# Kernel optimization log

Measured on AMD Instinct MI355X. Metric: run time of the kernel, lower is better.

The kernel has to match this reference:

```python
import jax, jax.numpy as jnp
import numpy as np

B, D = 65536, 512
EPS = 1e-15
MAXN = 1.0 - 4e-3  # geoopt fp32 ball boundary, c = 1


def _norm(x):
    return jnp.sqrt(jnp.clip(jnp.sum(x * x, -1, keepdims=True), EPS))


def _artanh(x):
    return jnp.arctanh(jnp.clip(x, -1.0 + 1e-7, 1.0 - 1e-7))


def projx(x):
    n = _norm(x)
    return jnp.where(n > MAXN, x / n * MAXN, x)


def mobius_add(x, y):
    x2 = jnp.sum(x * x, -1, keepdims=True)
    y2 = jnp.sum(y * y, -1, keepdims=True)
    xy = jnp.sum(x * y, -1, keepdims=True)
    num = (1.0 + 2.0 * xy + y2) * x + (1.0 - x2) * y
    den = 1.0 + 2.0 * xy + x2 * y2
    return num / jnp.maximum(den, EPS)


def expmap(x, u):
    un = _norm(u)
    lam = 2.0 / jnp.maximum(1.0 - jnp.sum(x * x, -1, keepdims=True), EPS)
    return mobius_add(x, jnp.tanh(lam * un / 2.0) * u / un)


def logmap(x, y):
    sub = mobius_add(-x, y)
    sn = _norm(sub)
    lam = 2.0 / jnp.maximum(1.0 - jnp.sum(x * x, -1, keepdims=True), EPS)
    return (2.0 / lam) * _artanh(sn) * sub / sn


def expmap0(u):
    un = _norm(u)
    return jnp.tanh(un) * u / un


def logmap0(y):
    yn = _norm(y)
    return _artanh(yn) * y / yn


def mobius_scalar_mul(r, x):
    xn = _norm(x)
    return jnp.tanh(r * _artanh(xn)) * x / xn


def poincare_fc(x, z, bias):
    # HNN++ Poincare fully-connected layer, c = 1
    zn = jnp.sqrt(jnp.clip(jnp.sum(z * z, 0), EPS))   # [out]
    z_unit = z / zn                                   # [in, out]
    two_r = 2.0 * bias                                # [out]
    cx2 = jnp.sum(x * x, -1, keepdims=True)           # [B, 1]
    inner = x @ z_unit                                # [B, out]
    v = 2.0 * zn * jnp.arcsinh(
        (2.0 * inner * jnp.cosh(two_r) - (1.0 + cx2) * jnp.sinh(two_r))
        / jnp.maximum(1.0 - cx2, EPS))
    w = jnp.sinh(v)
    return w / (1.0 + jnp.sqrt(1.0 + jnp.sum(w * w, -1, keepdims=True)))


def setup_inputs():
    key = jax.random.key(0)
    k1, k2, k3 = jax.random.split(key, 3)
    u1 = jax.random.normal(k1, (B, D), jnp.float32)
    u2 = jax.random.normal(k2, (B, D), jnp.float32)
    # points strictly inside the unit Poincare ball
    x_current = 0.7 * u1 / (1.0 + _norm(u1))
    x_previous = 0.7 * u2 / (1.0 + _norm(u2))
    # PoincareLinear id_init: 0.5*I, plus tiny noise so grads/outputs are non-degenerate
    z = 0.5 * jnp.eye(D, dtype=jnp.float32) + 0.01 * jax.random.normal(k3, (D, D), jnp.float32)
    bias = jnp.zeros((D,), jnp.float32)
    alpha = jnp.asarray(0.7, jnp.float32)
    step_size = jnp.asarray(1.0, jnp.float32)
    return {"x_current": x_current, "x_previous": x_previous, "z": z,
            "bias": bias, "alpha": alpha, "step_size": step_size}


def reference(x_current, x_previous, z, bias, alpha, step_size):
    # backward trajectory via logmap on the manifold (x_previous given)
    bt = logmap(x_previous, x_current)
    step = jax.nn.sigmoid(step_size)
    # PoincareLinear: expmap0 -> poincare_fc -> logmap0
    vel = logmap0(poincare_fc(expmap0(bt), z, bias))
    x_update = projx(expmap(x_current, step * vel))
    a = jax.nn.sigmoid(alpha)
    # poincare_residual_update
    xc = projx(x_current)
    xu = projx(x_update)
    x_next = projx(mobius_add(mobius_scalar_mul(a, xc), mobius_scalar_mul(1.0 - a, xu)))
    return (x_next, xc)
```

## Files before the change

### kernel.cpp

```cpp
#include <hip/hip_runtime.h>
#include <stdint.h>

#define DDIM 512
#define BROWS 65536
#define EPSF 1e-15f
#define MAXNF 0.996f
#define SQRT_EPSF 3.1622776e-8f
#define ATANH_CLIP 0.99999988f

typedef __bf16 bf16x8 __attribute__((ext_vector_type(8)));
typedef float f32x4 __attribute__((ext_vector_type(4)));

__device__ __forceinline__ unsigned short f2bf(float f) {
    union { float f; uint32_t u; } c; c.f = f;
    uint32_t u = c.u;
    u += 0x7fffu + ((u >> 16) & 1u);
    return (unsigned short)(u >> 16);
}

__device__ __forceinline__ float wred(float v) {
    v += __shfl_xor(v, 1);
    v += __shfl_xor(v, 2);
    v += __shfl_xor(v, 4);
    v += __shfl_xor(v, 8);
    v += __shfl_xor(v, 16);
    v += __shfl_xor(v, 32);
    return v;
}

__device__ __forceinline__ float fast_asinh(float t) {
    return __logf(t + sqrtf(fmaf(t, t, 1.0f)));
}
__device__ __forceinline__ float fast_sinh(float v) {
    float q = __expf(v);
    return 0.5f * (q - __builtin_amdgcn_rcpf(q));
}

__global__ void prep_kernel(const float* __restrict__ z, const float* __restrict__ bias,
                            float* __restrict__ znf, float* __restrict__ chv,
                            float* __restrict__ shv, unsigned short* __restrict__ zT) {
    int j = blockIdx.x;
    int l = threadIdx.x;
    float zv[8];
    float s = 0.f;
#pragma unroll
    for (int t = 0; t < 8; ++t) {
        float v = z[(size_t)(t * 64 + l) * DDIM + j];
        zv[t] = v;
        s = fmaf(v, v, s);
    }
    s = wred(s);
    float zn = sqrtf(fmaxf(s, EPSF));
    float inv = 1.0f / zn;
#pragma unroll
    for (int t = 0; t < 8; ++t)
        zT[(size_t)j * DDIM + t * 64 + l] = f2bf(zv[t] * inv);
    if (l == 0) {
        znf[j] = zn;
        float tr = 2.0f * bias[j];
        chv[j] = coshf(tr);
        shv[j] = sinhf(tr);
    }
}

__global__ __launch_bounds__(512, 2) void hpd_main(
    const float* __restrict__ Xc, const float* __restrict__ Xp,
    const float* __restrict__ znf, const float* __restrict__ chv, const float* __restrict__ shv,
    const unsigned short* __restrict__ zT,
    const float* __restrict__ alpha_p, const float* __restrict__ step_p,
    float* __restrict__ out)
{
    __shared__ __align__(16) unsigned char smem[98816];
    unsigned char* zbuf = smem + 65536;
    float* scx2 = (float*)(smem + 98304);
    float* sdcc = (float*)(smem + 98560);

    const int t = threadIdx.x;
    const int w = t >> 6;
    const int l = t & 63;
    const int l15 = l & 15;
    const int quad = l >> 4;
    const int r0 = blockIdx.x * 64;
    const size_t BDo = (size_t)BROWS * DDIM;

    float a_sig = 1.0f / (1.0f + __expf(-alpha_p[0]));
    float step_sig = 1.0f / (1.0f + __expf(-step_p[0]));

    float xcreg[8][8];
#pragma unroll
    for (int idx = 0; idx < 8; ++idx) {
        int row = (idx < 4) ? (w * 4 + idx) : (32 + w * 4 + (idx - 4));
        const float4* pc = (const float4*)(Xc + (size_t)(r0 + row) * DDIM + l * 8);
        const float4* pp = (const float4*)(Xp + (size_t)(r0 + row) * DDIM + l * 8);
        float4 c0 = pc[0], c1 = pc[1];
        float4 p0 = pp[0], p1 = pp[1];
        float xcv[8] = {c0.x, c0.y, c0.z, c0.w, c1.x, c1.y, c1.z, c1.w};
        float xpv[8] = {p0.x, p0.y, p0.z, p0.w, p1.x, p1.y, p1.z, p1.w};
        float dcc = 0.f, dpp = 0.f, dpc = 0.f;
#pragma unroll
        for (int j = 0; j < 8; ++j) {
            dcc = fmaf(xcv[j], xcv[j], dcc);
            dpp = fmaf(xpv[j], xpv[j], dpp);
            dpc = fmaf(xpv[j], xcv[j], dpc);
        }
        dcc = wred(dcc); dpp = wred(dpp); dpc = wred(dpc);
        float Ca = -(1.0f - 2.0f * dpc + dcc);
        float Cb = 1.0f - dpp;
        float den = fmaxf(1.0f - 2.0f * dpc + dpp * dcc, EPSF);
        float ssub = (Ca * Ca * dpp + 2.0f * Ca * Cb * dpc + Cb * Cb * dcc) / (den * den);
        float sn = sqrtf(fmaxf(ssub, EPSF));
        float tol = fmaxf(1.0f - dpp, EPSF);
        float art = atanhf(fminf(sn, ATANH_CLIP));
        float sbt = tol * art / sn;
        float un = fmaxf(tol * art, SQRT_EPSF);
        float te = tanhf(un);
        float se = te / un * sbt;
        float cep = se * Ca / den;
        float cex = se * Cb / den;
        if (l == 0) { scx2[row] = te * te; sdcc[row] = dcc; }
        unsigned short e8[8];
#pragma unroll
        for (int j = 0; j < 8; ++j) {
            e8[j] = f2bf(fmaf(cex, xcv[j], cep * xpv[j]));
            xcreg[idx][j] = xcv[j];
        }
        uint32_t u0 = (uint32_t)e8[0] | ((uint32_t)e8[1] << 16);
        uint32_t u1 = (uint32_t)e8[2] | ((uint32_t)e8[3] << 16);
        uint32_t u2 = (uint32_t)e8[4] | ((uint32_t)e8[5] << 16);
        uint32_t u3 = (uint32_t)e8[6] | ((uint32_t)e8[7] << 16);
        uint32_t off = row * 1024 + ((l ^ (row & 7)) * 16);
        *(uint4*)(smem + off) = make_uint4(u0, u1, u2, u3);
    }
    __syncthreads();

    f32x4 acc[4][4];
#pragma unroll
    for (int m = 0; m < 4; ++m)
#pragma unroll
        for (int j = 0; j < 4; ++j)
            acc[m][j] = (f32x4){0.f, 0.f, 0.f, 0.f};

#pragma unroll 1
    for (int ks = 0; ks < 16; ++ks) {
#pragma unroll
        for (int j = 0; j < 4; ++j) {
            int q = j * 512 + t;
            int n = q >> 2, c = q & 3;
            uint4 d = *(const uint4*)((const unsigned char*)zT + n * 1024 + ks * 64 + c * 16);
            int g = n >> 2;
            uint32_t off = g * 256 + (n & 3) * 16 + (((c + g) & 3) * 64);
            *(uint4*)(zbuf + off) = d;
        }
        __syncthreads();
        bf16x8 af[4], bfr[4];
#pragma unroll
        for (int m = 0; m < 4; ++m) {
            int row = m * 16 + l15;
            uint32_t off = row * 1024 + (((ks * 4 + quad) ^ (row & 7)) * 16);
            af[m] = *(const bf16x8*)(smem + off);
        }
#pragma unroll
        for (int j = 0; j < 4; ++j) {
            int n = w * 64 + j * 16 + l15;
            uint32_t off = (n >> 2) * 256 + (n & 3) * 16 + (((quad + (n >> 2)) & 3) * 64);
            bfr[j] = *(const bf16x8*)(zbuf + off);
        }
#pragma unroll
        for (int m = 0; m < 4; ++m)
#pragma unroll
            for (int j = 0; j < 4; ++j)
                acc[m][j] = __builtin_amdgcn_mfma_f32_16x16x32_bf16(af[m], bfr[j], acc[m][j], 0, 0, 0);
        __syncthreads();
    }

    float* stage = (float*)smem;
#pragma unroll
    for (int h = 0; h < 2; ++h) {
        __syncthreads();
#pragma unroll
        for (int mm = 0; mm < 2; ++mm) {
            int m = 2 * h + mm;
#pragma unroll
            for (int j = 0; j < 4; ++j) {
#pragma unroll
                for (int r = 0; r < 4; ++r) {
                    int rowl = mm * 16 + quad * 4 + r;
                    int n = w * 64 + j * 16 + l15;
                    stage[rowl * 512 + n] = acc[m][j][r];
                }
            }
        }
        __syncthreads();
#pragma unroll
        for (int i = 0; i < 4; ++i) {
            int rowl = w * 4 + i;
            int row = h * 32 + rowl;
            int idx = h * 4 + i;
            int grow = r0 + row;
            float4 in0 = *(const float4*)(stage + rowl * 512 + l * 8);
            float4 in1 = *(const float4*)(stage + rowl * 512 + l * 8 + 4);
            float inr[8] = {in0.x, in0.y, in0.z, in0.w, in1.x, in1.y, in1.z, in1.w};
            float4 zn0 = *(const float4*)(znf + l * 8);
            float4 zn1 = *(const float4*)(znf + l * 8 + 4);
            float4 ch0 = *(const float4*)(chv + l * 8);
            float4 ch1 = *(const float4*)(chv + l * 8 + 4);
            float4 sh0 = *(const float4*)(shv + l * 8);
            float4 sh1 = *(const float4*)(shv + l * 8 + 4);
            float znv[8] = {zn0.x, zn0.y, zn0.z, zn0.w, zn1.x, zn1.y, zn1.z, zn1.w};
            float chvv[8] = {ch0.x, ch0.y, ch0.z, ch0.w, ch1.x, ch1.y, ch1.z, ch1.w};
            float shvv[8] = {sh0.x, sh0.y, sh0.z, sh0.w, sh1.x, sh1.y, sh1.z, sh1.w};
            float cx2 = scx2[row], dcc = sdcc[row];
            float inv1m = 1.0f / fmaxf(1.0f - cx2, EPSF);
            float opc = 1.0f + cx2;
            float wv[8];
            float sw = 0.f, cw = 0.f;
#pragma unroll
            for (int j = 0; j < 8; ++j) {
                float arg = (2.0f * inr[j] * chvv[j] - opc * shvv[j]) * inv1m;
                float v = 2.0f * znv[j] * fast_asinh(arg);
                wv[j] = fast_sinh(v);
                sw = fmaf(wv[j], wv[j], sw);
                cw = fmaf(xcreg[idx][j], wv[j], cw);
            }
            sw = wred(sw); cw = wred(cw);
            float is = 1.0f / (1.0f + sqrtf(1.0f + sw));
            float nfc = sqrtf(fmaxf(sw * is * is, EPSF));
            float artf = atanhf(fminf(nfc, ATANH_CLIP));
            float un2 = fmaxf(step_sig * artf, SQRT_EPSF);
            float g = tanhf(un2 / fmaxf(1.0f - dcc, EPSF));
            float by = g * is / nfc;
            float xy = by * cw;
            float y2 = by * by * sw;
            float P = 1.0f + 2.0f * xy + y2;
            float den2 = fmaxf(1.0f + 2.0f * xy + dcc * y2, EPSF);
            float a1 = P / den2;
            float b1 = (1.0f - dcc) * by / den2;
            float s2u = a1 * a1 * dcc + 2.0f * a1 * b1 * cw + b1 * b1 * sw;
            float nxu = sqrtf(fmaxf(s2u, EPSF));
            float pj = (nxu > MAXNF) ? (MAXNF / nxu) : 1.0f;
            a1 *= pj; b1 *= pj;
            float nxu2 = fminf(nxu, MAXNF);
            float nx = sqrtf(fmaxf(dcc, EPSF));
            float sxc = (nx > MAXNF) ? (MAXNF / nx) : 1.0f;
            float nxc = fminf(nx, MAXNF);
            float A1 = tanhf(a_sig * atanhf(fminf(nxc, ATANH_CLIP))) / nxc * sxc;
            float t2s = tanhf((1.0f - a_sig) * atanhf(fminf(nxu2, ATANH_CLIP)));
            float sm2 = t2s / fmaxf(nxu2, SQRT_EPSF);
            float A2 = sm2 * a1, B2 = sm2 * b1;
            float x2m = A1 * A1 * dcc;
            float y2m = A2 * A2 * dcc + 2.0f * A2 * B2 * cw + B2 * B2 * sw;
            float xym = A1 * (A2 * dcc + B2 * cw);
            float num1 = 1.0f + 2.0f * xym + y2m;
            float num2 = 1.0f - x2m;
            float den3 = fmaxf(1.0f + 2.0f * xym + x2m * y2m, EPSF);
            float an = (num1 * A1 + num2 * A2) / den3;
            float bn = (num2 * B2) / den3;
            float s2n = an * an * dcc + 2.0f * an * bn * cw + bn * bn * sw;
            float nn = sqrtf(fmaxf(s2n, EPSF));
            float pj2 = (nn > MAXNF) ? (MAXNF / nn) : 1.0f;
            an *= pj2; bn *= pj2;
            float o0[8], o1[8];
#pragma unroll
            for (int j = 0; j < 8; ++j) {
                o0[j] = fmaf(an, xcreg[idx][j], bn * wv[j]);
                o1[j] = sxc * xcreg[idx][j];
            }
            float* p0 = out + (size_t)grow * DDIM + l * 8;
            float* p1 = out + BDo + (size_t)grow * DDIM + l * 8;
            *(float4*)(p0) = make_float4(o0[0], o0[1], o0[2], o0[3]);
            *(float4*)(p0 + 4) = make_float4(o0[4], o0[5], o0[6], o0[7]);
            *(float4*)(p1) = make_float4(o1[0], o1[1], o1[2], o1[3]);
            *(float4*)(p1 + 4) = make_float4(o1[4], o1[5], o1[6], o1[7]);
        }
    }
}

extern "C" void kernel_launch(void* const* d_in, const int* in_sizes, int n_in,
                              void* d_out, int out_size, void* d_ws, size_t ws_size,
                              hipStream_t stream) {
    const float* xc = (const float*)d_in[0];
    const float* xp = (const float*)d_in[1];
    const float* z = (const float*)d_in[2];
    const float* bias = (const float*)d_in[3];
    const float* alpha = (const float*)d_in[4];
    const float* stepsz = (const float*)d_in[5];
    float* out = (float*)d_out;

    float* znf = (float*)d_ws;
    float* chv = znf + 512;
    float* shv = znf + 1024;
    unsigned short* zT = (unsigned short*)(znf + 1536);

    prep_kernel<<<512, 64, 0, stream>>>(z, bias, znf, chv, shv, zT);
    hpd_main<<<BROWS / 64, 512, 0, stream>>>(xc, xp, znf, chv, shv, zT, alpha, stepsz, out);
}
```

Before: 631.9 us.

## Restructure epilogue in MFMA layout, load weights directly, drop z staging and registers

Drops the per-k-step shared-memory staging of the weight tile and its barriers, so each wave reads its bf16 B fragments straight from global (L2-resident) memory. The epilogue now works directly in the MFMA accumulator layout: row sums are reduced per wave, combined across waves in shared memory, and the per-row scalar math is done by 64 threads. Instead of holding x_current in registers, the epilogue re-reads it from global memory with strided scalar accesses, and the xc output is written early in the prologue. Fast tanh/atanh/reciprocal intrinsics replace the libm calls. Smaller LDS and fewer registers allow raising launch bounds to four blocks per CU. The trade-off is uncoalesced 4-byte global loads and stores in the epilogue, plus repeated global reads of z.

```diff
diff --git a/kernel.cpp b/kernel.cpp
--- a/kernel.cpp
+++ b/kernel.cpp
@@ -17,6 +17,8 @@
     u += 0x7fffu + ((u >> 16) & 1u);
     return (unsigned short)(u >> 16);
 }
+
+__device__ __forceinline__ float rcpf(float x) { return __builtin_amdgcn_rcpf(x); }
 
 __device__ __forceinline__ float wred(float v) {
     v += __shfl_xor(v, 1);
@@ -28,12 +30,21 @@
     return v;
 }
 
+__device__ __forceinline__ float fast_tanh_pos(float x) {
+    float t = __expf(-2.0f * x);
+    return (1.0f - t) * rcpf(1.0f + t);
+}
+__device__ __forceinline__ float fast_atanh_pos(float x) {
+    return 0.5f * __logf((1.0f + x) * rcpf(1.0f - x));
+}
 __device__ __forceinline__ float fast_asinh(float t) {
-    return __logf(t + sqrtf(fmaf(t, t, 1.0f)));
+    float a = fabsf(t);
+    float r = __logf(a + sqrtf(fmaf(a, a, 1.0f)));
+    return copysignf(r, t);
 }
 __device__ __forceinline__ float fast_sinh(float v) {
     float q = __expf(v);
-    return 0.5f * (q - __builtin_amdgcn_rcpf(q));
+    return 0.5f * (q - rcpf(q));
 }
 
 __global__ void prep_kernel(const float* __restrict__ z, const float* __restrict__ bias,
@@ -63,17 +74,20 @@
     }
 }
 
-__global__ __launch_bounds__(512, 2) void hpd_main(
+__global__ __launch_bounds__(512, 4) void hpd_main(
     const float* __restrict__ Xc, const float* __restrict__ Xp,
     const float* __restrict__ znf, const float* __restrict__ chv, const float* __restrict__ shv,
     const unsigned short* __restrict__ zT,
     const float* __restrict__ alpha_p, const float* __restrict__ step_p,
     float* __restrict__ out)
 {
-    __shared__ __align__(16) unsigned char smem[98816];
-    unsigned char* zbuf = smem + 65536;
-    float* scx2 = (float*)(smem + 98304);
-    float* sdcc = (float*)(smem + 98560);
+    __shared__ __align__(16) unsigned char smem[70656];
+    float* cx2s = (float*)(smem + 65536);
+    float* dccs = (float*)(smem + 65792);
+    float* swp  = (float*)(smem + 66048);
+    float* cwp  = (float*)(smem + 68096);
+    float* ans  = (float*)(smem + 70144);
+    float* bns  = (float*)(smem + 70400);
 
     const int t = threadIdx.x;
     const int w = t >> 6;
@@ -81,19 +95,19 @@
     const int l15 = l & 15;
     const int quad = l >> 4;
     const int r0 = blockIdx.x * 64;
-    const size_t BDo = (size_t)BROWS * DDIM;
-
-    float a_sig = 1.0f / (1.0f + __expf(-alpha_p[0]));
-    float step_sig = 1.0f / (1.0f + __expf(-step_p[0]));
-
-    float xcreg[8][8];
+
+    float a_sig = rcpf(1.0f + __expf(-alpha_p[0]));
+    float step_sig = rcpf(1.0f + __expf(-step_p[0]));
+
+    float* out1 = out + (size_t)BROWS * DDIM;
+
 #pragma unroll
     for (int idx = 0; idx < 8; ++idx) {
-        int row = (idx < 4) ? (w * 4 + idx) : (32 + w * 4 + (idx - 4));
-        const float4* pc = (const float4*)(Xc + (size_t)(r0 + row) * DDIM + l * 8);
-        const float4* pp = (const float4*)(Xp + (size_t)(r0 + row) * DDIM + l * 8);
-        float4 c0 = pc[0], c1 = pc[1];
-        float4 p0 = pp[0], p1 = pp[1];
+        int row = w * 4 + (idx & 3) + ((idx >> 2) << 5);
+        const float* pc = Xc + (size_t)(r0 + row) * DDIM + l * 8;
+        const float* pp = Xp + (size_t)(r0 + row) * DDIM + l * 8;
+        float4 c0 = *(const float4*)pc; float4 c1 = *(const float4*)(pc + 4);
+        float4 p0 = *(const float4*)pp; float4 p1 = *(const float4*)(pp + 4);
         float xcv[8] = {c0.x, c0.y, c0.z, c0.w, c1.x, c1.y, c1.z, c1.w};
         float xpv[8] = {p0.x, p0.y, p0.z, p0.w, p1.x, p1.y, p1.z, p1.w};
         float dcc = 0.f, dpp = 0.f, dpc = 0.f;
@@ -107,23 +121,27 @@
         float Ca = -(1.0f - 2.0f * dpc + dcc);
         float Cb = 1.0f - dpp;
         float den = fmaxf(1.0f - 2.0f * dpc + dpp * dcc, EPSF);
-        float ssub = (Ca * Ca * dpp + 2.0f * Ca * Cb * dpc + Cb * Cb * dcc) / (den * den);
+        float rden = rcpf(den);
+        float ssub = (Ca * Ca * dpp + 2.0f * Ca * Cb * dpc + Cb * Cb * dcc) * rden * rden;
         float sn = sqrtf(fmaxf(ssub, EPSF));
         float tol = fmaxf(1.0f - dpp, EPSF);
-        float art = atanhf(fminf(sn, ATANH_CLIP));
-        float sbt = tol * art / sn;
+        float art = fast_atanh_pos(fminf(sn, ATANH_CLIP));
+        float sbt = tol * art * rcpf(sn);
         float un = fmaxf(tol * art, SQRT_EPSF);
-        float te = tanhf(un);
-        float se = te / un * sbt;
-        float cep = se * Ca / den;
-        float cex = se * Cb / den;
-        if (l == 0) { scx2[row] = te * te; sdcc[row] = dcc; }
+        float te = fast_tanh_pos(un);
+        float se = te * rcpf(un) * sbt;
+        float cep = se * Ca * rden;
+        float cex = se * Cb * rden;
+        if (l == 0) { cx2s[row] = te * te; dccs[row] = dcc; }
+        float nx = sqrtf(fmaxf(dcc, EPSF));
+        float sxc = (nx > MAXNF) ? (MAXNF * rcpf(nx)) : 1.0f;
+        float* po1 = out1 + (size_t)(r0 + row) * DDIM + l * 8;
+        *(float4*)po1 = make_float4(sxc * xcv[0], sxc * xcv[1], sxc * xcv[2], sxc * xcv[3]);
+        *(float4*)(po1 + 4) = make_float4(sxc * xcv[4], sxc * xcv[5], sxc * xcv[6], sxc * xcv[7]);
         unsigned short e8[8];
 #pragma unroll
-        for (int j = 0; j < 8; ++j) {
+        for (int j = 0; j < 8; ++j)
             e8[j] = f2bf(fmaf(cex, xcv[j], cep * xpv[j]));
-            xcreg[idx][j] = xcv[j];
-        }
         uint32_t u0 = (uint32_t)e8[0] | ((uint32_t)e8[1] << 16);
         uint32_t u1 = (uint32_t)e8[2] | ((uint32_t)e8[3] << 16);
         uint32_t u2 = (uint32_t)e8[4] | ((uint32_t)e8[5] << 16);
@@ -140,137 +158,131 @@
         for (int j = 0; j < 4; ++j)
             acc[m][j] = (f32x4){0.f, 0.f, 0.f, 0.f};
 
+    const unsigned short* zbase = zT + (size_t)(w * 64 + l15) * DDIM + quad * 8;
 #pragma unroll 1
     for (int ks = 0; ks < 16; ++ks) {
-#pragma unroll
-        for (int j = 0; j < 4; ++j) {
-            int q = j * 512 + t;
-            int n = q >> 2, c = q & 3;
-            uint4 d = *(const uint4*)((const unsigned char*)zT + n * 1024 + ks * 64 + c * 16);
-            int g = n >> 2;
-            uint32_t off = g * 256 + (n & 3) * 16 + (((c + g) & 3) * 64);
-            *(uint4*)(zbuf + off) = d;
-        }
-        __syncthreads();
         bf16x8 af[4], bfr[4];
+#pragma unroll
+        for (int j = 0; j < 4; ++j)
+            bfr[j] = *(const bf16x8*)(zbase + (size_t)j * 16 * DDIM + ks * 32);
 #pragma unroll
         for (int m = 0; m < 4; ++m) {
             int row = m * 16 + l15;
-            uint32_t off = row * 1024 + (((ks * 4 + quad) ^ (row & 7)) * 16);
-            af[m] = *(const bf16x8*)(smem + off);
-        }
-#pragma unroll
-        for (int j = 0; j < 4; ++j) {
-            int n = w * 64 + j * 16 + l15;
-            uint32_t off = (n >> 2) * 256 + (n & 3) * 16 + (((quad + (n >> 2)) & 3) * 64);
-            bfr[j] = *(const bf16x8*)(zbuf + off);
+            af[m] = *(const bf16x8*)(smem + row * 1024 + (((ks * 4 + quad) ^ (row & 7)) * 16));
         }
 #pragma unroll
         for (int m = 0; m < 4; ++m)
 #pragma unroll
             for (int j = 0; j < 4; ++j)
                 acc[m][j] = __builtin_amdgcn_mfma_f32_16x16x32_bf16(af[m], bfr[j], acc[m][j], 0, 0, 0);
-        __syncthreads();
-    }
-
-    float* stage = (float*)smem;
-#pragma unroll
-    for (int h = 0; h < 2; ++h) {
-        __syncthreads();
-#pragma unroll
-        for (int mm = 0; mm < 2; ++mm) {
-            int m = 2 * h + mm;
-#pragma unroll
-            for (int j = 0; j < 4; ++j) {
-#pragma unroll
-                for (int r = 0; r < 4; ++r) {
-                    int rowl = mm * 16 + quad * 4 + r;
-                    int n = w * 64 + j * 16 + l15;
-                    stage[rowl * 512 + n] = acc[m][j][r];
-                }
+    }
+
+    float znv[4], chc[4], shc[4];
+#pragma unroll
+    for (int j = 0; j < 4; ++j) {
+        int col = w * 64 + j * 16 + l15;
+        znv[j] = znf[col]; chc[j] = chv[col]; shc[j] = shv[col];
+    }
+    const float* xb = Xc + (size_t)r0 * DDIM + w * 64 + l15;
+
+#pragma unroll
+    for (int m = 0; m < 4; ++m) {
+        int rbase = m * 16 + quad * 4;
+        float inv1m[4], opc[4];
+#pragma unroll
+        for (int r = 0; r < 4; ++r) {
+            float c2 = cx2s[rbase + r];
+            inv1m[r] = rcpf(fmaxf(1.0f - c2, EPSF));
+            opc[r] = 1.0f + c2;
+        }
+        float swr[4] = {0.f, 0.f, 0.f, 0.f}, cwr[4] = {0.f, 0.f, 0.f, 0.f};
+#pragma unroll
+        for (int j = 0; j < 4; ++j) {
+#pragma unroll
+            for (int r = 0; r < 4; ++r) {
+                float inner = acc[m][j][r];
+                float arg = fmaf(2.0f * inner, chc[j], -opc[r] * shc[j]) * inv1m[r];
+                float v = 2.0f * znv[j] * fast_asinh(arg);
+                float wv = fast_sinh(v);
+                acc[m][j][r] = wv;
+                float xv = xb[(size_t)(rbase + r) * DDIM + j * 16];
+                swr[r] = fmaf(wv, wv, swr[r]);
+                cwr[r] = fmaf(xv, wv, cwr[r]);
             }
         }
-        __syncthreads();
-#pragma unroll
-        for (int i = 0; i < 4; ++i) {
-            int rowl = w * 4 + i;
-            int row = h * 32 + rowl;
-            int idx = h * 4 + i;
-            int grow = r0 + row;
-            float4 in0 = *(const float4*)(stage + rowl * 512 + l * 8);
-            float4 in1 = *(const float4*)(stage + rowl * 512 + l * 8 + 4);
-            float inr[8] = {in0.x, in0.y, in0.z, in0.w, in1.x, in1.y, in1.z, in1.w};
-            float4 zn0 = *(const float4*)(znf + l * 8);
-            float4 zn1 = *(const float4*)(znf + l * 8 + 4);
-            float4 ch0 = *(const float4*)(chv + l * 8);
-            float4 ch1 = *(const float4*)(chv + l * 8 + 4);
-            float4 sh0 = *(const float4*)(shv + l * 8);
-            float4 sh1 = *(const float4*)(shv + l * 8 + 4);
-            float znv[8] = {zn0.x, zn0.y, zn0.z, zn0.w, zn1.x, zn1.y, zn1.z, zn1.w};
-            float chvv[8] = {ch0.x, ch0.y, ch0.z, ch0.w, ch1.x, ch1.y, ch1.z, ch1.w};
-            float shvv[8] = {sh0.x, sh0.y, sh0.z, sh0.w, sh1.x, sh1.y, sh1.z, sh1.w};
-            float cx2 = scx2[row], dcc = sdcc[row];
-            float inv1m = 1.0f / fmaxf(1.0f - cx2, EPSF);
-            float opc = 1.0f + cx2;
-            float wv[8];
-            float sw = 0.f, cw = 0.f;
-#pragma unroll
-            for (int j = 0; j < 8; ++j) {
-                float arg = (2.0f * inr[j] * chvv[j] - opc * shvv[j]) * inv1m;
-                float v = 2.0f * znv[j] * fast_asinh(arg);
-                wv[j] = fast_sinh(v);
-                sw = fmaf(wv[j], wv[j], sw);
-                cw = fmaf(xcreg[idx][j], wv[j], cw);
+#pragma unroll
+        for (int r = 0; r < 4; ++r) {
+            float s = swr[r], c = cwr[r];
+            s += __shfl_xor(s, 1); s += __shfl_xor(s, 2); s += __shfl_xor(s, 4); s += __shfl_xor(s, 8);
+            c += __shfl_xor(c, 1); c += __shfl_xor(c, 2); c += __shfl_xor(c, 4); c += __shfl_xor(c, 8);
+            if (l15 == 0) { swp[(rbase + r) * 8 + w] = s; cwp[(rbase + r) * 8 + w] = c; }
+        }
+    }
+    __syncthreads();
+
+    if (t < 64) {
+        int row = t;
+        float4 s0 = *(const float4*)(swp + row * 8);
+        float4 s1 = *(const float4*)(swp + row * 8 + 4);
+        float sw = ((s0.x + s0.y) + (s0.z + s0.w)) + ((s1.x + s1.y) + (s1.z + s1.w));
+        float4 q0 = *(const float4*)(cwp + row * 8);
+        float4 q1 = *(const float4*)(cwp + row * 8 + 4);
+        float cw = ((q0.x + q0.y) + (q0.z + q0.w)) + ((q1.x + q1.y) + (q1.z + q1.w));
+        float dcc = dccs[row];
+        float is = 1.0f / (1.0f + sqrtf(1.0f + sw));
+        float nfc = sqrtf(fmaxf(sw * is * is, EPSF));
+        float artf = fast_atanh_pos(fminf(nfc, ATANH_CLIP));
+        float un2 = fmaxf(step_sig * artf, SQRT_EPSF);
+        float g = fast_tanh_pos(un2 / fmaxf(1.0f - dcc, EPSF));
+        float by = g * is / nfc;
+        float xy = by * cw;
+        float y2 = by * by * sw;
+        float P = 1.0f + 2.0f * xy + y2;
+        float den2 = fmaxf(1.0f + 2.0f * xy + dcc * y2, EPSF);
+        float a1 = P / den2;
+        float b1 = (1.0f - dcc) * by / den2;
+        float s2u = a1 * a1 * dcc + 2.0f * a1 * b1 * cw + b1 * b1 * sw;
+        float nxu = sqrtf(fmaxf(s2u, EPSF));
+        float pj = (nxu > MAXNF) ? (MAXNF / nxu) : 1.0f;
+        a1 *= pj; b1 *= pj;
+        float nxu2 = fminf(nxu, MAXNF);
+        float nx = sqrtf(fmaxf(dcc, EPSF));
+        float sxc = (nx > MAXNF) ? (MAXNF / nx) : 1.0f;
+        float nxc = fminf(nx, MAXNF);
+        float A1 = fast_tanh_pos(a_sig * fast_atanh_pos(fminf(nxc, ATANH_CLIP))) / nxc * sxc;
+        float t2s = fast_tanh_pos((1.0f - a_sig) * fast_atanh_pos(fminf(nxu2, ATANH_CLIP)));
+        float sm2 = t2s / fmaxf(nxu2, SQRT_EPSF);
+        float A2 = sm2 * a1, B2 = sm2 * b1;
+        float x2m = A1 * A1 * dcc;
+        float y2m = A2 * A2 * dcc + 2.0f * A2 * B2 * cw + B2 * B2 * sw;
+        float xym = A1 * (A2 * dcc + B2 * cw);
+        float num1 = 1.0f + 2.0f * xym + y2m;
+        float num2 = 1.0f - x2m;
+        float den3 = fmaxf(1.0f + 2.0f * xym + x2m * y2m, EPSF);
+        float an = (num1 * A1 + num2 * A2) / den3;
+        float bn = (num2 * B2) / den3;
+        float s2n = an * an * dcc + 2.0f * an * bn * cw + bn * bn * sw;
+        float nn = sqrtf(fmaxf(s2n, EPSF));
+        float pj2 = (nn > MAXNF) ? (MAXNF / nn) : 1.0f;
+        ans[row] = an * pj2;
+        bns[row] = bn * pj2;
+    }
+    __syncthreads();
+
+    float* ob = out + (size_t)r0 * DDIM + w * 64 + l15;
+#pragma unroll
+    for (int m = 0; m < 4; ++m) {
+        int rbase = m * 16 + quad * 4;
+        float anv[4], bnv[4];
+#pragma unroll
+        for (int r = 0; r < 4; ++r) { anv[r] = ans[rbase + r]; bnv[r] = bns[rbase + r]; }
+#pragma unroll
+        for (int j = 0; j < 4; ++j) {
+#pragma unroll
+            for (int r = 0; r < 4; ++r) {
+                float xv = xb[(size_t)(rbase + r) * DDIM + j * 16];
+                ob[(size_t)(rbase + r) * DDIM + j * 16] = fmaf(anv[r], xv, bnv[r] * acc[m][j][r]);
             }
-            sw = wred(sw); cw = wred(cw);
-            float is = 1.0f / (1.0f + sqrtf(1.0f + sw));
-            float nfc = sqrtf(fmaxf(sw * is * is, EPSF));
-            float artf = atanhf(fminf(nfc, ATANH_CLIP));
-            float un2 = fmaxf(step_sig * artf, SQRT_EPSF);
-            float g = tanhf(un2 / fmaxf(1.0f - dcc, EPSF));
-            float by = g * is / nfc;
-            float xy = by * cw;
-            float y2 = by * by * sw;
-            float P = 1.0f + 2.0f * xy + y2;
-            float den2 = fmaxf(1.0f + 2.0f * xy + dcc * y2, EPSF);
-            float a1 = P / den2;
-            float b1 = (1.0f - dcc) * by / den2;
-            float s2u = a1 * a1 * dcc + 2.0f * a1 * b1 * cw + b1 * b1 * sw;
-            float nxu = sqrtf(fmaxf(s2u, EPSF));
-            float pj = (nxu > MAXNF) ? (MAXNF / nxu) : 1.0f;
-            a1 *= pj; b1 *= pj;
-            float nxu2 = fminf(nxu, MAXNF);
-            float nx = sqrtf(fmaxf(dcc, EPSF));
-            float sxc = (nx > MAXNF) ? (MAXNF / nx) : 1.0f;
-            float nxc = fminf(nx, MAXNF);
-            float A1 = tanhf(a_sig * atanhf(fminf(nxc, ATANH_CLIP))) / nxc * sxc;
-            float t2s = tanhf((1.0f - a_sig) * atanhf(fminf(nxu2, ATANH_CLIP)));
-            float sm2 = t2s / fmaxf(nxu2, SQRT_EPSF);
-            float A2 = sm2 * a1, B2 = sm2 * b1;
-            float x2m = A1 * A1 * dcc;
-            float y2m = A2 * A2 * dcc + 2.0f * A2 * B2 * cw + B2 * B2 * sw;
-            float xym = A1 * (A2 * dcc + B2 * cw);
-            float num1 = 1.0f + 2.0f * xym + y2m;
-            float num2 = 1.0f - x2m;
-            float den3 = fmaxf(1.0f + 2.0f * xym + x2m * y2m, EPSF);
-            float an = (num1 * A1 + num2 * A2) / den3;
-            float bn = (num2 * B2) / den3;
-            float s2n = an * an * dcc + 2.0f * an * bn * cw + bn * bn * sw;
-            float nn = sqrtf(fmaxf(s2n, EPSF));
-            float pj2 = (nn > MAXNF) ? (MAXNF / nn) : 1.0f;
-            an *= pj2; bn *= pj2;
-            float o0[8], o1[8];
-#pragma unroll
-            for (int j = 0; j < 8; ++j) {
-                o0[j] = fmaf(an, xcreg[idx][j], bn * wv[j]);
-                o1[j] = sxc * xcreg[idx][j];
-            }
-            float* p0 = out + (size_t)grow * DDIM + l * 8;
-            float* p1 = out + BDo + (size_t)grow * DDIM + l * 8;
-            *(float4*)(p0) = make_float4(o0[0], o0[1], o0[2], o0[3]);
-            *(float4*)(p0 + 4) = make_float4(o0[4], o0[5], o0[6], o0[7]);
-            *(float4*)(p1) = make_float4(o1[0], o1[1], o1[2], o1[3]);
-            *(float4*)(p1 + 4) = make_float4(o1[4], o1[5], o1[6], o1[7]);
         }
     }
 }
```

New measurement: 569.2 us. 9.9% less time.
